# Kernel tuning notes

Hardware: AMD Instinct MI355X
Metric: run time of the kernel (lower is better)

Reference implementation:

```python
import jax, jax.numpy as jnp
import numpy as np

B, S, D = 1, 2048, 2048
H, KV, HD = 16, 4, 128
E, TOPK, F = 8, 2, 2048
THETA = 500000.0
CLIP = 8.0
EPS = 1e-5


def setup_inputs() -> dict:
    key = jax.random.key(0)
    ks = jax.random.split(key, 8)
    sc = 0.02
    return {
        "hidden_states": jax.random.normal(ks[0], (B, S, D), jnp.float32),
        "position_ids": jnp.arange(S, dtype=jnp.int64)[None, :].repeat(B, axis=0),
        "ln1_w": jnp.ones((D,), jnp.float32),
        "ln2_w": jnp.ones((D,), jnp.float32),
        "wqkv": jax.random.normal(ks[1], (D, (H + 2 * KV) * HD), jnp.float32) * sc,
        "wo": jax.random.normal(ks[2], (H * HD, D), jnp.float32) * sc,
        "router_w": jax.random.normal(ks[3], (E, D), jnp.float32) * sc,
        "w1": jax.random.normal(ks[4], (E, D, F), jnp.float32) * sc,
        "v1": jax.random.normal(ks[5], (E, D, F), jnp.float32) * sc,
        "w2": jax.random.normal(ks[6], (E, F, D), jnp.float32) * sc,
    }


def _layernorm(x, w):
    mu = jnp.mean(x, axis=-1, keepdims=True)
    var = jnp.mean((x - mu) ** 2, axis=-1, keepdims=True)
    return (x - mu) * jax.lax.rsqrt(var + EPS) * w


def _rotate_half(x):
    x1, x2 = jnp.split(x, 2, axis=-1)
    return jnp.concatenate([-x2, x1], axis=-1)


def _rope(pos):
    inv_freq = 1.0 / (THETA ** (jnp.arange(0, HD, 2, dtype=jnp.float32) / HD))
    ang = pos.astype(jnp.float32)[..., None] * inv_freq  # [B,S,HD/2]
    ang = jnp.concatenate([ang, ang], axis=-1)  # [B,S,HD]
    return jnp.cos(ang)[:, None], jnp.sin(ang)[:, None]  # [B,1,S,HD]


def _forward(hidden_states, position_ids, ln1_w, ln2_w, wqkv, wo, router_w, w1, v1, w2):
    x = hidden_states
    # --- attention sublayer ---
    h = _layernorm(x, ln1_w)
    qkv = jnp.clip(h @ wqkv, -CLIP, CLIP)  # [B,S,(H+2KV)*HD]
    q, k, v = jnp.split(qkv, [H * HD, (H + KV) * HD], axis=-1)
    q = q.reshape(B, S, H, HD).transpose(0, 2, 1, 3)   # [B,H,S,HD]
    k = k.reshape(B, S, KV, HD).transpose(0, 2, 1, 3)  # [B,KV,S,HD]
    v = v.reshape(B, S, KV, HD).transpose(0, 2, 1, 3)
    cos, sin = _rope(position_ids)
    q = q * cos + _rotate_half(q) * sin
    k = k * cos + _rotate_half(k) * sin
    rep = H // KV
    k = jnp.repeat(k, rep, axis=1)  # [B,H,S,HD]
    v = jnp.repeat(v, rep, axis=1)
    scores = jnp.einsum("bhqd,bhkd->bhqk", q, k) / np.sqrt(HD).astype(np.float32)
    causal = jnp.tril(jnp.ones((S, S), bool))
    scores = jnp.where(causal, scores, jnp.finfo(scores.dtype).min)
    probs = jax.nn.softmax(scores, axis=-1)
    attn = jnp.einsum("bhqk,bhkd->bhqd", probs, v)
    attn = attn.transpose(0, 2, 1, 3).reshape(B, S, H * HD) @ wo
    x = x + attn
    # --- MoE FFN sublayer ---
    h = _layernorm(x, ln2_w).reshape(B * S, D)  # [T,D]
    logits = h @ router_w.T                      # [T,E]
    rp = jax.nn.softmax(logits, axis=-1)
    top_w, top_i = jax.lax.top_k(rp, TOPK)       # [T,K]
    top_w = top_w / jnp.sum(top_w, axis=-1, keepdims=True)
    T = B * S
    gate = jnp.zeros((T, E), h.dtype).at[jnp.arange(T)[:, None], top_i].add(top_w)
    g = jax.nn.silu(jnp.einsum("td,edf->tef", h, w1)) * jnp.einsum("td,edf->tef", h, v1)
    y = jnp.einsum("tef,efd,te->td", g, w2, gate)
    x = x + y.reshape(B, S, D)
    return x


def reference(hidden_states, position_ids, ln1_w, ln2_w, wqkv, wo, router_w, w1, v1, w2):
    return _forward(hidden_states, position_ids, ln1_w, ln2_w, wqkv, wo, router_w, w1, v1, w2)
```

## Files before the change

kernel.cpp:

```cpp
#include <hip/hip_runtime.h>

#define S_LEN 2048
#define DMODEL 2048
#define NH 16
#define NKV 4
#define HD 128
#define NE 8
#define FF 2048
#define QKV_N 3072

typedef __attribute__((ext_vector_type(8))) short short8;
typedef __attribute__((ext_vector_type(4))) float f32x4;

__device__ inline unsigned short f2bf(float f) {
  unsigned int u = __builtin_bit_cast(unsigned int, f);
  u += 0x7fffu + ((u >> 16) & 1u);
  return (unsigned short)(u >> 16);
}
__device__ inline float bf2f(unsigned short h) {
  unsigned int u = ((unsigned int)h) << 16;
  return __builtin_bit_cast(float, u);
}
__device__ inline void split2(float v, unsigned short& h, unsigned short& l) {
  h = f2bf(v);
  l = f2bf(v - bf2f(h));
}


__device__ inline void stage_rows(const unsigned short* __restrict__ src, int ld,
                                  long row0, int k0, unsigned short* dst) {
  int t = threadIdx.x;
  int r = t >> 2, q = t & 3;
  int s = (r ^ (r >> 2)) & 3;
  uint4 v0 = *(const uint4*)(src + (size_t)(row0 + r) * ld + k0 + q * 8);
  uint4 v1 = *(const uint4*)(src + (size_t)(row0 + r + 64) * ld + k0 + q * 8);
  *(uint4*)(dst + r * 32 + ((q ^ s) << 3)) = v0;
  *(uint4*)(dst + (r + 64) * 32 + ((q ^ s) << 3)) = v1;
}

__device__ inline void loadA2_rows(const unsigned short* __restrict__ src, int ld,
                                   long row0, int k0, uint4 va[2]) {
  int t = threadIdx.x;
  int r = t >> 2, q = t & 3;
  va[0] = *(const uint4*)(src + (size_t)(row0 + r) * ld + k0 + q * 8);
  va[1] = *(const uint4*)(src + (size_t)(row0 + r + 64) * ld + k0 + q * 8);
}
__device__ inline void loadA2_g(const unsigned short* __restrict__ src, int ld,
                                const int* __restrict__ toks, int nvalid, int k0,
                                uint4 va[2]) {
  int t = threadIdx.x;
  int r = t >> 2, q = t & 3;
#pragma unroll
  for (int rr = 0; rr < 2; rr++) {
    int row = r + rr * 64;
    uint4 v = make_uint4(0, 0, 0, 0);
    if (row < nvalid) v = *(const uint4*)(src + (size_t)toks[row] * ld + k0 + q * 8);
    va[rr] = v;
  }
}
__device__ inline void writeA2(const uint4 va[2], unsigned short* dst) {
  int t = threadIdx.x;
  int r = t >> 2, q = t & 3;
  int s = (r ^ (r >> 2)) & 3;
  *(uint4*)(dst + r * 32 + ((q ^ s) << 3)) = va[0];
  *(uint4*)(dst + (r + 64) * 32 + ((q ^ s) << 3)) = va[1];
}

__device__ inline void gload16(const void* g, void* l) {
  __builtin_amdgcn_global_load_lds((const __attribute__((address_space(1))) unsigned int*)g,
                                   (__attribute__((address_space(3))) unsigned int*)l,
                                   16, 0, 0);
}
__device__ inline void stageB_chunk(const unsigned short* __restrict__ chunk,
                                    unsigned short* __restrict__ lds) {
  int w = threadIdx.x >> 6, l = threadIdx.x & 63;
  const unsigned short* s = chunk + w * 1024 + l * 8;
  unsigned short* d = lds + w * 1024;
  gload16(s, d);
  gload16(s + 512, d + 512);
}

#define WAIT_ALL  asm volatile("s_waitcnt vmcnt(0) lgkmcnt(0)" ::: "memory")
#define WAIT_LDS  asm volatile("s_waitcnt lgkmcnt(0)" ::: "memory")
#define SCHEDBAR  __builtin_amdgcn_sched_barrier(0)
#define BAR       __builtin_amdgcn_s_barrier()


__device__ inline void mma16(const unsigned short* As, const unsigned short* Bs,
                             int wr, int wc, f32x4 acc[4][4]) {
  int l = threadIdx.x & 63;
  int lr = l & 15, lg = l >> 4;
  int qoff = ((lg ^ ((lr ^ (lr >> 2)) & 3)) << 3);
  short8 a[4], b[4];
#pragma unroll
  for (int m = 0; m < 4; m++)
    a[m] = *(const short8*)(As + (wr + m * 16 + lr) * 32 + qoff);
#pragma unroll
  for (int n = 0; n < 4; n++)
    b[n] = *(const short8*)(Bs + (wc + n * 16 + lr) * 32 + qoff);
#pragma unroll
  for (int m = 0; m < 4; m++)
#pragma unroll
    for (int n = 0; n < 4; n++)
      acc[m][n] = __builtin_amdgcn_mfma_f32_16x16x32_bf16(a[m], b[n], acc[m][n], 0, 0, 0);
}

__device__ inline void mma16_dualB(const unsigned short* As, const unsigned short* Bs1,
                                   const unsigned short* Bs2, int wr, int wc,
                                   f32x4 acc1[4][4], f32x4 acc2[4][4]) {
  int l = threadIdx.x & 63;
  int lr = l & 15, lg = l >> 4;
  int qoff = ((lg ^ ((lr ^ (lr >> 2)) & 3)) << 3);
  short8 a[4], b1[4], b2[4];
#pragma unroll
  for (int m = 0; m < 4; m++)
    a[m] = *(const short8*)(As + (wr + m * 16 + lr) * 32 + qoff);
#pragma unroll
  for (int n = 0; n < 4; n++) {
    b1[n] = *(const short8*)(Bs1 + (wc + n * 16 + lr) * 32 + qoff);
    b2[n] = *(const short8*)(Bs2 + (wc + n * 16 + lr) * 32 + qoff);
  }
#pragma unroll
  for (int m = 0; m < 4; m++)
#pragma unroll
    for (int n = 0; n < 4; n++) {
      acc1[m][n] = __builtin_amdgcn_mfma_f32_16x16x32_bf16(a[m], b1[n], acc1[m][n], 0, 0, 0);
      acc2[m][n] = __builtin_amdgcn_mfma_f32_16x16x32_bf16(a[m], b2[n], acc2[m][n], 0, 0, 0);
    }
}

__device__ inline void mma16_split_reg(const unsigned short* Ash, const unsigned short* Asl,
                                       const unsigned short* Bsh, const unsigned short* Bsl,
                                       int wr, int wc, f32x4 acc[4][4]) {
  int l = threadIdx.x & 63;
  int lr = l & 15, lg = l >> 4;
  int qoff = ((lg ^ ((lr ^ (lr >> 2)) & 3)) << 3);
  short8 ah[4], al[4], bh[4], bl[4];
#pragma unroll
  for (int m = 0; m < 4; m++) {
    ah[m] = *(const short8*)(Ash + (wr + m * 16 + lr) * 32 + qoff);
    al[m] = *(const short8*)(Asl + (wr + m * 16 + lr) * 32 + qoff);
  }
#pragma unroll
  for (int n = 0; n < 4; n++) {
    bh[n] = *(const short8*)(Bsh + (wc + n * 16 + lr) * 32 + qoff);
    bl[n] = *(const short8*)(Bsl + (wc + n * 16 + lr) * 32 + qoff);
  }
#pragma unroll
  for (int m = 0; m < 4; m++)
#pragma unroll
    for (int n = 0; n < 4; n++) {
      acc[m][n] = __builtin_amdgcn_mfma_f32_16x16x32_bf16(ah[m], bh[n], acc[m][n], 0, 0, 0);
      acc[m][n] = __builtin_amdgcn_mfma_f32_16x16x32_bf16(ah[m], bl[n], acc[m][n], 0, 0, 0);
      acc[m][n] = __builtin_amdgcn_mfma_f32_16x16x32_bf16(al[m], bh[n], acc[m][n], 0, 0, 0);
    }
}


__global__ __launch_bounds__(256) void k_pack1(const float* __restrict__ src, long ld,
                                               long zs, int nc,
                                               unsigned short* __restrict__ dst) {
  __shared__ float tile[32][132];
  const float* Sp = src + (long)blockIdx.z * zs;
  int c = blockIdx.x, t = threadIdx.x;
  for (int i = 0; i < 4; i++) {
    int kt = blockIdx.y * 4 + i;
    long k0 = (long)kt * 32, n0 = (long)c * 128;
    {
      int k = t >> 3, nn = (t & 7) * 16;
      const float4* p = (const float4*)(Sp + (k0 + k) * ld + n0 + nn);
#pragma unroll
      for (int j = 0; j < 4; j++) *(float4*)&tile[k][nn + j * 4] = p[j];
    }
    __syncthreads();
    size_t cbase = ((size_t)(blockIdx.z * nc + c) * 64 + kt) * 4096;
#pragma unroll
    for (int uu = 0; uu < 2; uu++) {
      int u = t * 2 + uu;
      int n = u >> 2, qp = u & 3;
      int q = qp ^ ((n ^ (n >> 2)) & 3);
      unsigned short hb[8] __attribute__((aligned(16)));
#pragma unroll
      for (int j = 0; j < 8; j++) hb[j] = f2bf(tile[8 * q + j][n]);
      *(uint4*)(dst + cbase + u * 8) = *(const uint4*)hb;
    }
    __syncthreads();
  }
}

__global__ __launch_bounds__(256) void k_pack2(const float* __restrict__ src, long ld,
                                               long zs, int nc,
                                               unsigned short* __restrict__ dh,
                                               unsigned short* __restrict__ dl) {
  __shared__ float tile[32][132];
  const float* Sp = src + (long)blockIdx.z * zs;
  int c = blockIdx.x, t = threadIdx.x;
  for (int i = 0; i < 4; i++) {
    int kt = blockIdx.y * 4 + i;
    long k0 = (long)kt * 32, n0 = (long)c * 128;
    {
      int k = t >> 3, nn = (t & 7) * 16;
      const float4* p = (const float4*)(Sp + (k0 + k) * ld + n0 + nn);
#pragma unroll
      for (int j = 0; j < 4; j++) *(float4*)&tile[k][nn + j * 4] = p[j];
    }
    __syncthreads();
    size_t cbase = ((size_t)(blockIdx.z * nc + c) * 64 + kt) * 4096;
#pragma unroll
    for (int uu = 0; uu < 2; uu++) {
      int u = t * 2 + uu;
      int n = u >> 2, qp = u & 3;
      int q = qp ^ ((n ^ (n >> 2)) & 3);
      unsigned short hb[8] __attribute__((aligned(16)));
      unsigned short lb[8] __attribute__((aligned(16)));
#pragma unroll
      for (int j = 0; j < 8; j++) split2(tile[8 * q + j][n], hb[j], lb[j]);
      *(uint4*)(dh + cbase + u * 8) = *(const uint4*)hb;
      *(uint4*)(dl + cbase + u * 8) = *(const uint4*)lb;
    }
    __syncthreads();
  }
}

__global__ __launch_bounds__(256) void k_packbf(const unsigned short* __restrict__ src,
                                                unsigned short* __restrict__ dst) {
  int ttile = blockIdx.x;
  int z = blockIdx.y;
  const unsigned short* Sp = src + ((size_t)z * S_LEN + (size_t)ttile * 128) * HD;
  size_t ob = ((size_t)z * 64 + (size_t)ttile * 4) * 4096;
  int t = threadIdx.x;
#pragma unroll
  for (int kst = 0; kst < 4; kst++) {
#pragma unroll
    for (int uu = 0; uu < 2; uu++) {
      int u = t * 2 + uu;
      int n = u >> 2, qp = u & 3;
      int q = qp ^ ((n ^ (n >> 2)) & 3);
      *(uint4*)(dst + ob + (size_t)kst * 4096 + u * 8) =
          *(const uint4*)(Sp + (size_t)n * HD + kst * 32 + q * 8);
    }
  }
}


__global__ __launch_bounds__(256) void k_qkv_s(const unsigned short* __restrict__ Ah,
                                               const unsigned short* __restrict__ Al,
                                               const unsigned short* __restrict__ BPh,
                                               const unsigned short* __restrict__ BPl,
                                               float* __restrict__ C) {
  __shared__ unsigned short Ash[2 * 4096], Asl[2 * 4096], Bsh[2 * 4096], Bsl[2 * 4096];
  int row0 = blockIdx.y * 128;
  size_t cb = (size_t)blockIdx.x * 64 * 4096;
  int w = threadIdx.x >> 6;
  int wr = (w >> 1) * 64, wc = (w & 1) * 64;
  uint4 vah[2], val[2];
  loadA2_rows(Ah, DMODEL, row0, 0, vah);
  loadA2_rows(Al, DMODEL, row0, 0, val);
  stageB_chunk(BPh + cb, Bsh);
  stageB_chunk(BPl + cb, Bsl);
  writeA2(vah, Ash);
  writeA2(val, Asl);
  WAIT_ALL;
  BAR;
  f32x4 acc[4][4] = {};
  for (int kt = 0; kt < 64; kt++) {
    int cur = (kt & 1) << 12, nxt = 4096 - cur;
    if (kt + 1 < 64) {
      loadA2_rows(Ah, DMODEL, row0, (kt + 1) * 32, vah);
      loadA2_rows(Al, DMODEL, row0, (kt + 1) * 32, val);
      stageB_chunk(BPh + cb + (size_t)(kt + 1) * 4096, Bsh + nxt);
      stageB_chunk(BPl + cb + (size_t)(kt + 1) * 4096, Bsl + nxt);
    }
    SCHEDBAR;
    mma16_split_reg(Ash + cur, Asl + cur, Bsh + cur, Bsl + cur, wr, wc, acc);
    SCHEDBAR;
    if (kt + 1 < 64) {
      writeA2(vah, Ash + nxt);
      writeA2(val, Asl + nxt);
    }
    WAIT_ALL;
    BAR;
  }
  int col0 = blockIdx.x * 128;
  int l = threadIdx.x & 63;
  int er = wr + ((l >> 4) << 2), ec = wc + (l & 15);
#pragma unroll
  for (int m = 0; m < 4; m++)
#pragma unroll
    for (int n = 0; n < 4; n++)
#pragma unroll
      for (int r = 0; r < 4; r++) {
        float v = acc[m][n][r];
        v = fminf(fmaxf(v, -8.f), 8.f);
        C[(size_t)(row0 + er + m * 16 + r) * QKV_N + col0 + ec + n * 16] = v;
      }
}

__global__ __launch_bounds__(256) void k_wo_s(const unsigned short* __restrict__ Ah,
                                              const unsigned short* __restrict__ Al,
                                              const unsigned short* __restrict__ BPh,
                                              const unsigned short* __restrict__ BPl,
                                              const float* __restrict__ resid,
                                              float* __restrict__ x1) {
  __shared__ unsigned short Ash[2 * 4096], Asl[2 * 4096], Bsh[2 * 4096], Bsl[2 * 4096];
  int row0 = blockIdx.y * 128;
  size_t cb = (size_t)blockIdx.x * 64 * 4096;
  int w = threadIdx.x >> 6;
  int wr = (w >> 1) * 64, wc = (w & 1) * 64;
  uint4 vah[2], val[2];
  loadA2_rows(Ah, DMODEL, row0, 0, vah);
  loadA2_rows(Al, DMODEL, row0, 0, val);
  stageB_chunk(BPh + cb, Bsh);
  stageB_chunk(BPl + cb, Bsl);
  writeA2(vah, Ash);
  writeA2(val, Asl);
  WAIT_ALL;
  BAR;
  f32x4 acc[4][4] = {};
  for (int kt = 0; kt < 64; kt++) {
    int cur = (kt & 1) << 12, nxt = 4096 - cur;
    if (kt + 1 < 64) {
      loadA2_rows(Ah, DMODEL, row0, (kt + 1) * 32, vah);
      loadA2_rows(Al, DMODEL, row0, (kt + 1) * 32, val);
      stageB_chunk(BPh + cb + (size_t)(kt + 1) * 4096, Bsh + nxt);
      stageB_chunk(BPl + cb + (size_t)(kt + 1) * 4096, Bsl + nxt);
    }
    SCHEDBAR;
    mma16_split_reg(Ash + cur, Asl + cur, Bsh + cur, Bsl + cur, wr, wc, acc);
    SCHEDBAR;
    if (kt + 1 < 64) {
      writeA2(vah, Ash + nxt);
      writeA2(val, Asl + nxt);
    }
    WAIT_ALL;
    BAR;
  }
  int col0 = blockIdx.x * 128;
  int l = threadIdx.x & 63;
  int er = wr + ((l >> 4) << 2), ec = wc + (l & 15);
#pragma unroll
  for (int m = 0; m < 4; m++)
#pragma unroll
    for (int n = 0; n < 4; n++)
#pragma unroll
      for (int r = 0; r < 4; r++) {
        size_t idx = (size_t)(row0 + er + m * 16 + r) * DMODEL + col0 + ec + n * 16;
        x1[idx] = resid[idx] + acc[m][n][r];
      }
}


__global__ __launch_bounds__(128) void k_flash(const unsigned short* __restrict__ qh,
                                               const unsigned short* __restrict__ ql,
                                               const unsigned short* __restrict__ kPh,
                                               const unsigned short* __restrict__ kPl,
                                               const unsigned short* __restrict__ vPh,
                                               const unsigned short* __restrict__ vPl,
                                               unsigned short* __restrict__ ath,
                                               unsigned short* __restrict__ atl) {
  int bid = blockIdx.x;
  int h = (bid & 7) | ((bid >> 8) << 3);
  int rt = (bid >> 3) & 31;
  int kv = h >> 2;
  int ntiles = (rt >> 1) + 1;
  __shared__ float Pds[2][32 * 132];
  int t = threadIdx.x;
  int w = t >> 6, l = t & 63;
  int lr = l & 15, lg = l >> 4;
  int qoff = ((lg ^ ((lr ^ (lr >> 2)) & 3)) << 3);
  int wrow0 = rt * 64 + w * 32;
  const unsigned short* Qbh = qh + (size_t)h * S_LEN * HD;
  const unsigned short* Qbl = ql + (size_t)h * S_LEN * HD;
  const unsigned short* Kch = kPh + (size_t)kv * 64 * 4096;
  const unsigned short* Kcl = kPl + (size_t)kv * 64 * 4096;
  const unsigned short* Vch = vPh + (size_t)kv * 64 * 4096;
  const unsigned short* Vcl = vPl + (size_t)kv * 64 * 4096;
  float* Pw = &Pds[w][0];
  float mrun[2][4], lrun[2][4];
  f32x4 Oc[2][8];
#pragma unroll
  for (int m = 0; m < 2; m++)
#pragma unroll
    for (int r = 0; r < 4; r++) { mrun[m][r] = -3.4e38f; lrun[m][r] = 0.f; }
#pragma unroll
  for (int m = 0; m < 2; m++)
#pragma unroll
    for (int n = 0; n < 8; n++)
#pragma unroll
      for (int r = 0; r < 4; r++) Oc[m][n][r] = 0.f;
  const float scale = 0.08838834764831845f;

  for (int kt = 0; kt < ntiles; kt++) {
    f32x4 Sa[2][8];
#pragma unroll
    for (int m = 0; m < 2; m++)
#pragma unroll
      for (int n = 0; n < 8; n++)
#pragma unroll
        for (int r = 0; r < 4; r++) Sa[m][n][r] = 0.f;
#pragma unroll
    for (int kst = 0; kst < 4; kst++) {
      short8 qfh[2], qfl[2];
#pragma unroll
      for (int m = 0; m < 2; m++) {
        size_t o = (size_t)(wrow0 + m * 16 + lr) * HD + kst * 32 + lg * 8;
        qfh[m] = *(const short8*)(Qbh + o);
        qfl[m] = *(const short8*)(Qbl + o);
      }
      const unsigned short* Kh = Kch + (size_t)(kt * 4 + kst) * 4096;
      const unsigned short* Kl = Kcl + (size_t)(kt * 4 + kst) * 4096;
      short8 bh[8], bl[8];
#pragma unroll
      for (int n = 0; n < 8; n++) {
        bh[n] = *(const short8*)(Kh + (n * 16 + lr) * 32 + qoff);
        bl[n] = *(const short8*)(Kl + (n * 16 + lr) * 32 + qoff);
      }
#pragma unroll
      for (int m = 0; m < 2; m++)
#pragma unroll
        for (int n = 0; n < 8; n++) {
          Sa[m][n] = __builtin_amdgcn_mfma_f32_16x16x32_bf16(qfh[m], bh[n], Sa[m][n], 0, 0, 0);
          Sa[m][n] = __builtin_amdgcn_mfma_f32_16x16x32_bf16(qfh[m], bl[n], Sa[m][n], 0, 0, 0);
          Sa[m][n] = __builtin_amdgcn_mfma_f32_16x16x32_bf16(qfl[m], bh[n], Sa[m][n], 0, 0, 0);
        }
    }
#pragma unroll
    for (int m = 0; m < 2; m++)
#pragma unroll
      for (int r = 0; r < 4; r++) {
        int row = wrow0 + m * 16 + lg * 4 + r;
        float mx = mrun[m][r];
#pragma unroll
        for (int n = 0; n < 8; n++) {
          float v = Sa[m][n][r] * scale;
          int col = kt * 128 + n * 16 + lr;
          v = (col <= row) ? v : -3.4e38f;
          Sa[m][n][r] = v;
          mx = fmaxf(mx, v);
        }
        mx = fmaxf(mx, __shfl_xor(mx, 1));
        mx = fmaxf(mx, __shfl_xor(mx, 2));
        mx = fmaxf(mx, __shfl_xor(mx, 4));
        mx = fmaxf(mx, __shfl_xor(mx, 8));
        float al_ = expf(mrun[m][r] - mx);
        float sum = 0.f;
#pragma unroll
        for (int n = 0; n < 8; n++) {
          float v = Sa[m][n][r];
          float e = (v > -1.0e37f) ? expf(v - mx) : 0.f;
          Sa[m][n][r] = e;
          sum += e;
        }
        sum += __shfl_xor(sum, 1);
        sum += __shfl_xor(sum, 2);
        sum += __shfl_xor(sum, 4);
        sum += __shfl_xor(sum, 8);
        lrun[m][r] = lrun[m][r] * al_ + sum;
        mrun[m][r] = mx;
#pragma unroll
        for (int n = 0; n < 8; n++) Oc[m][n][r] *= al_;
      }
    WAIT_LDS;
    SCHEDBAR;
#pragma unroll
    for (int m = 0; m < 2; m++)
#pragma unroll
      for (int n = 0; n < 8; n++)
#pragma unroll
        for (int r = 0; r < 4; r++)
          Pw[(m * 16 + lg * 4 + r) * 132 + n * 16 + lr] = Sa[m][n][r];
    WAIT_LDS;
    SCHEDBAR;
#pragma unroll
    for (int kst = 0; kst < 4; kst++) {
      const unsigned short* Vh = Vch + (size_t)(kt * 4 + kst) * 4096;
      const unsigned short* Vl = Vcl + (size_t)(kt * 4 + kst) * 4096;
      short8 bh[8], bl[8];
#pragma unroll
      for (int n = 0; n < 8; n++) {
        bh[n] = *(const short8*)(Vh + (n * 16 + lr) * 32 + qoff);
        bl[n] = *(const short8*)(Vl + (n * 16 + lr) * 32 + qoff);
      }
#pragma unroll
      for (int m = 0; m < 2; m++) {
        const float* pp = &Pw[(m * 16 + lr) * 132 + kst * 32 + lg * 8];
        unsigned short ahb[8] __attribute__((aligned(16)));
        unsigned short alb[8] __attribute__((aligned(16)));
#pragma unroll
        for (int j = 0; j < 8; j++) split2(pp[j], ahb[j], alb[j]);
        short8 ah = *(const short8*)ahb;
        short8 al_ = *(const short8*)alb;
#pragma unroll
        for (int n = 0; n < 8; n++) {
          Oc[m][n] = __builtin_amdgcn_mfma_f32_16x16x32_bf16(ah, bh[n], Oc[m][n], 0, 0, 0);
          Oc[m][n] = __builtin_amdgcn_mfma_f32_16x16x32_bf16(ah, bl[n], Oc[m][n], 0, 0, 0);
          Oc[m][n] = __builtin_amdgcn_mfma_f32_16x16x32_bf16(al_, bh[n], Oc[m][n], 0, 0, 0);
        }
      }
    }
  }
#pragma unroll
  for (int m = 0; m < 2; m++)
#pragma unroll
    for (int r = 0; r < 4; r++) {
      size_t row = wrow0 + m * 16 + lg * 4 + r;
      float lv = lrun[m][r];
#pragma unroll
      for (int n = 0; n < 8; n++) {
        unsigned short hh, ll;
        split2(Oc[m][n][r] / lv, hh, ll);
        size_t o = row * DMODEL + (size_t)h * HD + n * 16 + lr;
        ath[o] = hh;
        atl[o] = ll;
      }
    }
}


__global__ __launch_bounds__(256) void k_moe1f(const unsigned short* __restrict__ h2b,
                                               const unsigned short* __restrict__ wPa,
                                               const unsigned short* __restrict__ wPb,
                                               const int* __restrict__ off,
                                               const int* __restrict__ ptok,
                                               const int* __restrict__ meta,
                                               unsigned short* __restrict__ g) {
  int ty = blockIdx.y;
  if (ty >= meta[25]) return;
  int tt = meta[26 + ty];
  int e = tt & 7, m0 = tt >> 3;
  int nvalid = min(128, meta[e] - m0);
  const int* toks = ptok + off[e] + m0;
  const unsigned short* B1 = wPa + (size_t)(e * 16 + blockIdx.x) * 64 * 4096;
  const unsigned short* B2 = wPb + (size_t)(e * 16 + blockIdx.x) * 64 * 4096;
  __shared__ unsigned short As[2 * 4096], Bs1[2 * 4096], Bs2[2 * 4096];
  int w = threadIdx.x >> 6;
  int wr = (w >> 1) * 64, wc = (w & 1) * 64;
  uint4 va[2];
  loadA2_g(h2b, DMODEL, toks, nvalid, 0, va);
  stageB_chunk(B1, Bs1);
  stageB_chunk(B2, Bs2);
  writeA2(va, As);
  WAIT_ALL;
  BAR;
  f32x4 acc1[4][4] = {}, acc2[4][4] = {};
  for (int kt = 0; kt < 64; kt++) {
    int cur = (kt & 1) << 12, nxt = 4096 - cur;
    if (kt + 1 < 64) {
      loadA2_g(h2b, DMODEL, toks, nvalid, (kt + 1) * 32, va);
      stageB_chunk(B1 + (size_t)(kt + 1) * 4096, Bs1 + nxt);
      stageB_chunk(B2 + (size_t)(kt + 1) * 4096, Bs2 + nxt);
    }
    SCHEDBAR;
    mma16_dualB(As + cur, Bs1 + cur, Bs2 + cur, wr, wc, acc1, acc2);
    SCHEDBAR;
    if (kt + 1 < 64) writeA2(va, As + nxt);
    WAIT_ALL;
    BAR;
  }
  int col0 = blockIdx.x * 128;
  int l = threadIdx.x & 63;
  int er = wr + ((l >> 4) << 2), ec = wc + (l & 15);
  size_t gbase = (size_t)off[e] + m0;
#pragma unroll
  for (int m = 0; m < 4; m++)
#pragma unroll
    for (int n = 0; n < 4; n++)
#pragma unroll
      for (int r = 0; r < 4; r++) {
        int rl = er + m * 16 + r;
        if (rl < nvalid) {
          float a = acc1[m][n][r];
          float s = a / (1.f + expf(-a));
          g[(gbase + rl) * FF + col0 + ec + n * 16] = f2bf(s * acc2[m][n][r]);
        }
      }
}

__global__ __launch_bounds__(256) void k_moe2(const unsigned short* __restrict__ g,
                                              const unsigned short* __restrict__ wP,
                                              const int* __restrict__ off,
                                              const int* __restrict__ ptok,
                                              const float* __restrict__ pw,
                                              const int* __restrict__ meta,
                                              float* __restrict__ y) {
  int ty = blockIdx.y;
  if (ty >= meta[25]) return;
  int tt = meta[26 + ty];
  int e = tt & 7, m0 = tt >> 3;
  int nvalid = min(128, meta[e] - m0);
  long pbase = (long)off[e] + m0;
  const unsigned short* Bb = wP + (size_t)(e * 16 + blockIdx.x) * 64 * 4096;
  __shared__ unsigned short As[2 * 4096], Bs[2 * 4096];
  int w = threadIdx.x >> 6;
  int wr = (w >> 1) * 64, wc = (w & 1) * 64;
  uint4 va[2];
  loadA2_rows(g, FF, pbase, 0, va);
  stageB_chunk(Bb, Bs);
  writeA2(va, As);
  WAIT_ALL;
  BAR;
  f32x4 acc[4][4] = {};
  for (int kt = 0; kt < 64; kt++) {
    int cur = (kt & 1) << 12, nxt = 4096 - cur;
    if (kt + 1 < 64) {
      loadA2_rows(g, FF, pbase, (kt + 1) * 32, va);
      stageB_chunk(Bb + (size_t)(kt + 1) * 4096, Bs + nxt);
    }
    SCHEDBAR;
    mma16(As + cur, Bs + cur, wr, wc, acc);
    SCHEDBAR;
    if (kt + 1 < 64) writeA2(va, As + nxt);
    WAIT_ALL;
    BAR;
  }
  int col0 = blockIdx.x * 128;
  int l = threadIdx.x & 63;
  int er = wr + ((l >> 4) << 2), ec = wc + (l & 15);
#pragma unroll
  for (int m = 0; m < 4; m++)
#pragma unroll
    for (int n = 0; n < 4; n++)
#pragma unroll
      for (int r = 0; r < 4; r++) {
        int rl = er + m * 16 + r;
        if (rl < nvalid) {
          long p = pbase + rl;
          int tk = ptok[p];
          atomicAdd(&y[(size_t)tk * DMODEL + col0 + ec + n * 16], acc[m][n][r] * pw[p]);
        }
      }
}


__global__ __launch_bounds__(256) void k_ln(const float* __restrict__ x,
                                            const float* __restrict__ w,
                                            unsigned short* __restrict__ obh,
                                            unsigned short* __restrict__ obl,
                                            float* __restrict__ of) {
  int row = blockIdx.x;
  const float* xr = x + (size_t)row * DMODEL;
  float s = 0.f, ss = 0.f;
  for (int c = threadIdx.x; c < DMODEL; c += 256) {
    float v = xr[c];
    s += v; ss += v * v;
  }
#pragma unroll
  for (int o = 32; o; o >>= 1) { s += __shfl_down(s, o); ss += __shfl_down(ss, o); }
  __shared__ float rs[4], rss[4], mu_s, inv_s;
  int wid = threadIdx.x >> 6;
  if ((threadIdx.x & 63) == 0) { rs[wid] = s; rss[wid] = ss; }
  __syncthreads();
  if (threadIdx.x == 0) {
    float S1 = rs[0] + rs[1] + rs[2] + rs[3];
    float S2 = rss[0] + rss[1] + rss[2] + rss[3];
    float mu = S1 / DMODEL;
    mu_s = mu;
    inv_s = rsqrtf(S2 / DMODEL - mu * mu + 1e-5f);
  }
  __syncthreads();
  float mu = mu_s, inv = inv_s;
  for (int c = threadIdx.x; c < DMODEL; c += 256) {
    float v = (xr[c] - mu) * inv * w[c];
    unsigned short hh, ll;
    split2(v, hh, ll);
    obh[(size_t)row * DMODEL + c] = hh;
    if (obl) obl[(size_t)row * DMODEL + c] = ll;
    if (of) of[(size_t)row * DMODEL + c] = v;
  }
}

__global__ void k_rope2(const float* __restrict__ qkv, unsigned short* __restrict__ qh,
                        unsigned short* __restrict__ ql, unsigned short* __restrict__ kh,
                        unsigned short* __restrict__ kl) {
  int t = blockIdx.x;
  int d = threadIdx.x;
  float pf = (float)pow(500000.0, (double)d * (1.0 / 64.0));
  float invf = 1.0f / pf;
  float ang = (float)t * invf;
  float cs = (float)cos((double)ang);
  float sn = (float)sin((double)ang);
  const float* row = qkv + (size_t)t * QKV_N;
  unsigned short hh, ll;
#pragma unroll
  for (int hq = 0; hq < NH; hq++) {
    float a = row[hq * HD + d], b = row[hq * HD + d + 64];
    size_t base = ((size_t)hq * S_LEN + t) * HD;
    split2(a * cs - b * sn, hh, ll); qh[base + d] = hh; ql[base + d] = ll;
    split2(b * cs + a * sn, hh, ll); qh[base + d + 64] = hh; ql[base + d + 64] = ll;
  }
#pragma unroll
  for (int kv = 0; kv < NKV; kv++) {
    float a = row[NH * HD + kv * HD + d], b = row[NH * HD + kv * HD + d + 64];
    size_t base = ((size_t)kv * S_LEN + t) * HD;
    split2(a * cs - b * sn, hh, ll); kh[base + d] = hh; kl[base + d] = ll;
    split2(b * cs + a * sn, hh, ll); kh[base + d + 64] = hh; kl[base + d + 64] = ll;
  }
}

__global__ __launch_bounds__(256) void k_router(const float* __restrict__ h2,
                                                const float* __restrict__ rw,
                                                int* __restrict__ topi,
                                                float* __restrict__ topw,
                                                int* __restrict__ cnt) {
  int t = blockIdx.x;
  __shared__ float hs[DMODEL];
  __shared__ float lg[NE];
  for (int c = threadIdx.x; c < DMODEL; c += 256) hs[c] = h2[(size_t)t * DMODEL + c];
  __syncthreads();
  int grp = threadIdx.x >> 5;
  int ln = threadIdx.x & 31;
  float p = 0.f;
  for (int c = ln; c < DMODEL; c += 32) p += hs[c] * rw[(size_t)grp * DMODEL + c];
#pragma unroll
  for (int o = 16; o; o >>= 1) p += __shfl_down(p, o, 32);
  if (ln == 0) lg[grp] = p;
  __syncthreads();
  if (threadIdx.x == 0) {
    float l0 = -3.4e38f; int i0 = 0;
    for (int e = 0; e < NE; e++)
      if (lg[e] > l0) { l0 = lg[e]; i0 = e; }
    float l1 = -3.4e38f; int i1 = 0;
    for (int e = 0; e < NE; e++)
      if (e != i0 && lg[e] > l1) { l1 = lg[e]; i1 = e; }
    float z = expf(l1 - l0);
    topi[t * 2] = i0; topi[t * 2 + 1] = i1;
    topw[t * 2] = 1.f / (1.f + z); topw[t * 2 + 1] = z / (1.f + z);
    atomicAdd(&cnt[i0], 1);
    atomicAdd(&cnt[i1], 1);
  }
}

__global__ void k_scan(int* __restrict__ meta) {
  if (threadIdx.x == 0 && blockIdx.x == 0) {
    int o = 0, nt = 0;
    for (int e = 0; e < NE; e++) {
      meta[16 + e] = o;
      for (int m0 = 0; m0 < meta[e]; m0 += 128) meta[26 + nt++] = (m0 << 3) | e;
      o += meta[e];
    }
    meta[24] = o;
    meta[25] = nt;
  }
}

__global__ void k_fill(const int* __restrict__ topi, const float* __restrict__ topw,
                       int* __restrict__ meta, int* __restrict__ ptok,
                       float* __restrict__ pw) {
  int t = blockIdx.x * blockDim.x + threadIdx.x;
  if (t >= S_LEN) return;
#pragma unroll
  for (int j = 0; j < 2; j++) {
    int e = topi[t * 2 + j];
    int p = atomicAdd(&meta[8 + e], 1);
    ptok[meta[16 + e] + p] = t;
    pw[meta[16 + e] + p] = topw[t * 2 + j];
  }
}

__global__ void k_final(float* __restrict__ out, const float* __restrict__ y) {
  int i = blockIdx.x * blockDim.x + threadIdx.x;
  float4 a = ((const float4*)out)[i];
  float4 b = ((const float4*)y)[i];
  ((float4*)out)[i] = make_float4(a.x + b.x, a.y + b.y, a.z + b.z, a.w + b.w);
}


extern "C" void kernel_launch(void* const* d_in, const int* in_sizes, int n_in,
                              void* d_out, int out_size, void* d_ws, size_t ws_size,
                              hipStream_t stream) {
  (void)in_sizes; (void)n_in; (void)out_size; (void)ws_size;
  const float* x = (const float*)d_in[0];
  const float* ln1w = (const float*)d_in[2];
  const float* ln2w = (const float*)d_in[3];
  const float* wqkv = (const float*)d_in[4];
  const float* wo = (const float*)d_in[5];
  const float* rw = (const float*)d_in[6];
  const float* w1 = (const float*)d_in[7];
  const float* v1 = (const float*)d_in[8];
  const float* w2 = (const float*)d_in[9];
  float* out = (float*)d_out;

  char* wsb = (char*)d_ws;
  const size_t MiB = 1u << 20;
  unsigned short* h1h = (unsigned short*)(wsb + 0 * MiB);
  unsigned short* h1l = (unsigned short*)(wsb + 8 * MiB);
  float* qkvb = (float*)(wsb + 16 * MiB);
  unsigned short* qh = (unsigned short*)(wsb + 40 * MiB);
  unsigned short* ql = (unsigned short*)(wsb + 48 * MiB);
  unsigned short* kh = (unsigned short*)(wsb + 56 * MiB);
  unsigned short* kl = (unsigned short*)(wsb + 58 * MiB);
  unsigned short* vPh = (unsigned short*)(wsb + 60 * MiB);
  unsigned short* vPl = (unsigned short*)(wsb + 62 * MiB);
  unsigned short* kPh = (unsigned short*)(wsb + 64 * MiB);
  unsigned short* kPl = (unsigned short*)(wsb + 66 * MiB);
  unsigned short* ath = (unsigned short*)(wsb + 68 * MiB);
  unsigned short* atl = (unsigned short*)(wsb + 76 * MiB);
  unsigned short* wqkvPh = (unsigned short*)(wsb + 84 * MiB);
  unsigned short* wqkvPl = (unsigned short*)(wsb + 96 * MiB);
  unsigned short* woPh = (unsigned short*)(wsb + 108 * MiB);
  unsigned short* woPl = (unsigned short*)(wsb + 116 * MiB);
  float* h2f = (float*)(wsb + 0 * MiB);
  unsigned short* h2b = (unsigned short*)(wsb + 16 * MiB);
  unsigned short* g = (unsigned short*)(wsb + 24 * MiB);
  float* y = (float*)(wsb + 40 * MiB);
  unsigned short* wPa = (unsigned short*)(wsb + 56 * MiB);
  unsigned short* wPb = (unsigned short*)(wsb + 120 * MiB);
  char* small = wsb + 184 * MiB;
  int* topi = (int*)small;
  float* topw = (float*)(small + 16384);
  int* ptok = (int*)(small + 32768);
  float* pw = (float*)(small + 49152);
  int* meta = (int*)(small + 65536);

  k_pack2<<<dim3(QKV_N / 128, 16, 1), 256, 0, stream>>>(wqkv, QKV_N, 0, QKV_N / 128,
                                                        wqkvPh, wqkvPl);
  k_pack2<<<dim3(DMODEL / 128, 16, 1), 256, 0, stream>>>(wo, DMODEL, 0, DMODEL / 128,
                                                         woPh, woPl);

  k_ln<<<S_LEN, 256, 0, stream>>>(x, ln1w, h1h, h1l, (float*)nullptr);
  k_qkv_s<<<dim3(QKV_N / 128, S_LEN / 128), 256, 0, stream>>>(h1h, h1l, wqkvPh, wqkvPl, qkvb);
  k_rope2<<<S_LEN, 64, 0, stream>>>(qkvb, qh, ql, kh, kl);
  k_pack2<<<dim3(1, 16, NKV), 256, 0, stream>>>(qkvb + (NH + NKV) * HD, QKV_N, HD, 1,
                                                vPh, vPl);
  k_packbf<<<dim3(16, NKV), 256, 0, stream>>>(kh, kPh);
  k_packbf<<<dim3(16, NKV), 256, 0, stream>>>(kl, kPl);
  k_flash<<<512, 128, 0, stream>>>(qh, ql, kPh, kPl, vPh, vPl, ath, atl);
  k_wo_s<<<dim3(16, 16), 256, 0, stream>>>(ath, atl, woPh, woPl, x, out);

  k_ln<<<S_LEN, 256, 0, stream>>>(out, ln2w, h2b, (unsigned short*)nullptr, h2f);
  hipMemsetAsync(y, 0, (size_t)S_LEN * DMODEL * 4, stream);
  hipMemsetAsync(meta, 0, 512, stream);
  k_router<<<S_LEN, 256, 0, stream>>>(h2f, rw, topi, topw, meta);
  k_scan<<<1, 64, 0, stream>>>(meta);
  k_fill<<<8, 256, 0, stream>>>(topi, topw, meta, ptok, pw);
  k_pack1<<<dim3(16, 16, NE), 256, 0, stream>>>(w1, FF, (long)DMODEL * FF, 16, wPa);
  k_pack1<<<dim3(16, 16, NE), 256, 0, stream>>>(v1, FF, (long)DMODEL * FF, 16, wPb);
  k_moe1f<<<dim3(16, 40), 256, 0, stream>>>(h2b, wPa, wPb, meta + 16, ptok, meta, g);
  k_pack1<<<dim3(16, 16, NE), 256, 0, stream>>>(w2, DMODEL, (long)FF * DMODEL, 16, wPa);
  k_moe2<<<dim3(16, 40), 256, 0, stream>>>(g, wPa, meta + 16, ptok, pw, meta, y);
  k_final<<<(S_LEN * DMODEL / 4) / 256, 256, 0, stream>>>(out, y);
}
```

Before: 971.8 us.

## Pre-pack GEMM A operands into swizzled tiles and fold MoE output into residual

LayerNorm and flash attention now write their split bf16 outputs straight into the tiled, swizzled layout the GEMMs use. A new gather kernel packs routed tokens the same way, so every GEMM can stage A through direct global-to-LDS loads instead of register loads followed by LDS writes. The MoE GEMMs drop double buffering for a single buffer with two barriers per k-step. The second expert GEMM now atomically adds into the output, which removes the y memset and the final add kernel. In exchange there is an extra gather pass, a redundant second LayerNorm launch, and less load/compute overlap in the MoE loops.

```diff
diff --git a/kernel.cpp b/kernel.cpp
--- a/kernel.cpp
+++ b/kernel.cpp
@@ -26,45 +26,6 @@
   l = f2bf(v - bf2f(h));
 }
 
-
-__device__ inline void stage_rows(const unsigned short* __restrict__ src, int ld,
-                                  long row0, int k0, unsigned short* dst) {
-  int t = threadIdx.x;
-  int r = t >> 2, q = t & 3;
-  int s = (r ^ (r >> 2)) & 3;
-  uint4 v0 = *(const uint4*)(src + (size_t)(row0 + r) * ld + k0 + q * 8);
-  uint4 v1 = *(const uint4*)(src + (size_t)(row0 + r + 64) * ld + k0 + q * 8);
-  *(uint4*)(dst + r * 32 + ((q ^ s) << 3)) = v0;
-  *(uint4*)(dst + (r + 64) * 32 + ((q ^ s) << 3)) = v1;
-}
-
-__device__ inline void loadA2_rows(const unsigned short* __restrict__ src, int ld,
-                                   long row0, int k0, uint4 va[2]) {
-  int t = threadIdx.x;
-  int r = t >> 2, q = t & 3;
-  va[0] = *(const uint4*)(src + (size_t)(row0 + r) * ld + k0 + q * 8);
-  va[1] = *(const uint4*)(src + (size_t)(row0 + r + 64) * ld + k0 + q * 8);
-}
-__device__ inline void loadA2_g(const unsigned short* __restrict__ src, int ld,
-                                const int* __restrict__ toks, int nvalid, int k0,
-                                uint4 va[2]) {
-  int t = threadIdx.x;
-  int r = t >> 2, q = t & 3;
-#pragma unroll
-  for (int rr = 0; rr < 2; rr++) {
-    int row = r + rr * 64;
-    uint4 v = make_uint4(0, 0, 0, 0);
-    if (row < nvalid) v = *(const uint4*)(src + (size_t)toks[row] * ld + k0 + q * 8);
-    va[rr] = v;
-  }
-}
-__device__ inline void writeA2(const uint4 va[2], unsigned short* dst) {
-  int t = threadIdx.x;
-  int r = t >> 2, q = t & 3;
-  int s = (r ^ (r >> 2)) & 3;
-  *(uint4*)(dst + r * 32 + ((q ^ s) << 3)) = va[0];
-  *(uint4*)(dst + (r + 64) * 32 + ((q ^ s) << 3)) = va[1];
-}
 
 __device__ inline void gload16(const void* g, void* l) {
   __builtin_amdgcn_global_load_lds((const __attribute__((address_space(1))) unsigned int*)g,
@@ -242,46 +203,66 @@
   }
 }
 
-
-__global__ __launch_bounds__(256) void k_qkv_s(const unsigned short* __restrict__ Ah,
-                                               const unsigned short* __restrict__ Al,
+__global__ __launch_bounds__(256) void k_gpack(const unsigned short* __restrict__ h2b,
+                                               const int* __restrict__ ptok,
+                                               const int* __restrict__ meta,
+                                               unsigned short* __restrict__ hAP) {
+  int ty = blockIdx.x;
+  if (ty >= meta[25]) return;
+  int tt = meta[26 + ty];
+  int e = tt & 7, m0 = tt >> 3;
+  int nvalid = min(128, meta[e] - m0);
+  const int* toks = ptok + meta[16 + e] + m0;
+  int t = threadIdx.x;
+  int r = t >> 2, q = t & 3;
+  int s = (r ^ (r >> 2)) & 3;
+  for (int kt = blockIdx.y * 8; kt < blockIdx.y * 8 + 8; kt++) {
+    unsigned short* dst = hAP + ((size_t)ty * 64 + kt) * 4096;
+#pragma unroll
+    for (int rr = 0; rr < 2; rr++) {
+      int row = r + rr * 64;
+      uint4 v = make_uint4(0, 0, 0, 0);
+      if (row < nvalid)
+        v = *(const uint4*)(h2b + (size_t)toks[row] * DMODEL + kt * 32 + q * 8);
+      *(uint4*)(dst + row * 32 + ((q ^ s) << 3)) = v;
+    }
+  }
+}
+
+
+__global__ __launch_bounds__(256) void k_qkv_s(const unsigned short* __restrict__ APh,
+                                               const unsigned short* __restrict__ APl,
                                                const unsigned short* __restrict__ BPh,
                                                const unsigned short* __restrict__ BPl,
                                                float* __restrict__ C) {
   __shared__ unsigned short Ash[2 * 4096], Asl[2 * 4096], Bsh[2 * 4096], Bsl[2 * 4096];
-  int row0 = blockIdx.y * 128;
+  size_t ab = (size_t)blockIdx.y * 64 * 4096;
   size_t cb = (size_t)blockIdx.x * 64 * 4096;
   int w = threadIdx.x >> 6;
   int wr = (w >> 1) * 64, wc = (w & 1) * 64;
-  uint4 vah[2], val[2];
-  loadA2_rows(Ah, DMODEL, row0, 0, vah);
-  loadA2_rows(Al, DMODEL, row0, 0, val);
+  stageB_chunk(APh + ab, Ash);
+  stageB_chunk(APl + ab, Asl);
   stageB_chunk(BPh + cb, Bsh);
   stageB_chunk(BPl + cb, Bsl);
-  writeA2(vah, Ash);
-  writeA2(val, Asl);
   WAIT_ALL;
   BAR;
   f32x4 acc[4][4] = {};
   for (int kt = 0; kt < 64; kt++) {
     int cur = (kt & 1) << 12, nxt = 4096 - cur;
     if (kt + 1 < 64) {
-      loadA2_rows(Ah, DMODEL, row0, (kt + 1) * 32, vah);
-      loadA2_rows(Al, DMODEL, row0, (kt + 1) * 32, val);
-      stageB_chunk(BPh + cb + (size_t)(kt + 1) * 4096, Bsh + nxt);
-      stageB_chunk(BPl + cb + (size_t)(kt + 1) * 4096, Bsl + nxt);
+      size_t o = (size_t)(kt + 1) * 4096;
+      stageB_chunk(APh + ab + o, Ash + nxt);
+      stageB_chunk(APl + ab + o, Asl + nxt);
+      stageB_chunk(BPh + cb + o, Bsh + nxt);
+      stageB_chunk(BPl + cb + o, Bsl + nxt);
     }
     SCHEDBAR;
     mma16_split_reg(Ash + cur, Asl + cur, Bsh + cur, Bsl + cur, wr, wc, acc);
     SCHEDBAR;
-    if (kt + 1 < 64) {
-      writeA2(vah, Ash + nxt);
-      writeA2(val, Asl + nxt);
-    }
     WAIT_ALL;
     BAR;
   }
-  int col0 = blockIdx.x * 128;
+  int row0 = blockIdx.y * 128, col0 = blockIdx.x * 128;
   int l = threadIdx.x & 63;
   int er = wr + ((l >> 4) << 2), ec = wc + (l & 15);
 #pragma unroll
@@ -296,46 +277,40 @@
       }
 }
 
-__global__ __launch_bounds__(256) void k_wo_s(const unsigned short* __restrict__ Ah,
-                                              const unsigned short* __restrict__ Al,
+__global__ __launch_bounds__(256) void k_wo_s(const unsigned short* __restrict__ APh,
+                                              const unsigned short* __restrict__ APl,
                                               const unsigned short* __restrict__ BPh,
                                               const unsigned short* __restrict__ BPl,
                                               const float* __restrict__ resid,
                                               float* __restrict__ x1) {
   __shared__ unsigned short Ash[2 * 4096], Asl[2 * 4096], Bsh[2 * 4096], Bsl[2 * 4096];
-  int row0 = blockIdx.y * 128;
+  size_t ab = (size_t)blockIdx.y * 64 * 4096;
   size_t cb = (size_t)blockIdx.x * 64 * 4096;
   int w = threadIdx.x >> 6;
   int wr = (w >> 1) * 64, wc = (w & 1) * 64;
-  uint4 vah[2], val[2];
-  loadA2_rows(Ah, DMODEL, row0, 0, vah);
-  loadA2_rows(Al, DMODEL, row0, 0, val);
+  stageB_chunk(APh + ab, Ash);
+  stageB_chunk(APl + ab, Asl);
   stageB_chunk(BPh + cb, Bsh);
   stageB_chunk(BPl + cb, Bsl);
-  writeA2(vah, Ash);
-  writeA2(val, Asl);
   WAIT_ALL;
   BAR;
   f32x4 acc[4][4] = {};
   for (int kt = 0; kt < 64; kt++) {
     int cur = (kt & 1) << 12, nxt = 4096 - cur;
     if (kt + 1 < 64) {
-      loadA2_rows(Ah, DMODEL, row0, (kt + 1) * 32, vah);
-      loadA2_rows(Al, DMODEL, row0, (kt + 1) * 32, val);
-      stageB_chunk(BPh + cb + (size_t)(kt + 1) * 4096, Bsh + nxt);
-      stageB_chunk(BPl + cb + (size_t)(kt + 1) * 4096, Bsl + nxt);
+      size_t o = (size_t)(kt + 1) * 4096;
+      stageB_chunk(APh + ab + o, Ash + nxt);
+      stageB_chunk(APl + ab + o, Asl + nxt);
+      stageB_chunk(BPh + cb + o, Bsh + nxt);
+      stageB_chunk(BPl + cb + o, Bsl + nxt);
     }
     SCHEDBAR;
     mma16_split_reg(Ash + cur, Asl + cur, Bsh + cur, Bsl + cur, wr, wc, acc);
     SCHEDBAR;
-    if (kt + 1 < 64) {
-      writeA2(vah, Ash + nxt);
-      writeA2(val, Asl + nxt);
-    }
     WAIT_ALL;
     BAR;
   }
-  int col0 = blockIdx.x * 128;
+  int row0 = blockIdx.y * 128, col0 = blockIdx.x * 128;
   int l = threadIdx.x & 63;
   int er = wr + ((l >> 4) << 2), ec = wc + (l & 15);
 #pragma unroll
@@ -356,8 +331,8 @@
                                                const unsigned short* __restrict__ kPl,
                                                const unsigned short* __restrict__ vPh,
                                                const unsigned short* __restrict__ vPl,
-                                               unsigned short* __restrict__ ath,
-                                               unsigned short* __restrict__ atl) {
+                                               unsigned short* __restrict__ atPh,
+                                               unsigned short* __restrict__ atPl) {
   int bid = blockIdx.x;
   int h = (bid & 7) | ((bid >> 8) << 3);
   int rt = (bid >> 3) & 31;
@@ -503,25 +478,27 @@
   for (int m = 0; m < 2; m++)
 #pragma unroll
     for (int r = 0; r < 4; r++) {
-      size_t row = wrow0 + m * 16 + lg * 4 + r;
+      int row = wrow0 + m * 16 + lg * 4 + r;
+      int rtc = row >> 7, rl = row & 127;
+      int sr = (rl ^ (rl >> 2)) & 3;
       float lv = lrun[m][r];
 #pragma unroll
       for (int n = 0; n < 8; n++) {
+        int col = h * HD + n * 16 + lr;
+        size_t off = ((size_t)(rtc * 64 + (col >> 5))) * 4096 + rl * 32 +
+                     ((((col & 31) >> 3) ^ sr) << 3) + (col & 7);
         unsigned short hh, ll;
         split2(Oc[m][n][r] / lv, hh, ll);
-        size_t o = row * DMODEL + (size_t)h * HD + n * 16 + lr;
-        ath[o] = hh;
-        atl[o] = ll;
-      }
-    }
-}
-
-
-__global__ __launch_bounds__(256) void k_moe1f(const unsigned short* __restrict__ h2b,
+        atPh[off] = hh;
+        atPl[off] = ll;
+      }
+    }
+}
+
+
+__global__ __launch_bounds__(256) void k_moe1f(const unsigned short* __restrict__ hAP,
                                                const unsigned short* __restrict__ wPa,
                                                const unsigned short* __restrict__ wPb,
-                                               const int* __restrict__ off,
-                                               const int* __restrict__ ptok,
                                                const int* __restrict__ meta,
                                                unsigned short* __restrict__ g) {
   int ty = blockIdx.y;
@@ -529,38 +506,25 @@
   int tt = meta[26 + ty];
   int e = tt & 7, m0 = tt >> 3;
   int nvalid = min(128, meta[e] - m0);
-  const int* toks = ptok + off[e] + m0;
+  const unsigned short* Ab = hAP + (size_t)ty * 64 * 4096;
   const unsigned short* B1 = wPa + (size_t)(e * 16 + blockIdx.x) * 64 * 4096;
   const unsigned short* B2 = wPb + (size_t)(e * 16 + blockIdx.x) * 64 * 4096;
-  __shared__ unsigned short As[2 * 4096], Bs1[2 * 4096], Bs2[2 * 4096];
+  __shared__ unsigned short As[4096], Bs1[4096], Bs2[4096];
   int w = threadIdx.x >> 6;
   int wr = (w >> 1) * 64, wc = (w & 1) * 64;
-  uint4 va[2];
-  loadA2_g(h2b, DMODEL, toks, nvalid, 0, va);
-  stageB_chunk(B1, Bs1);
-  stageB_chunk(B2, Bs2);
-  writeA2(va, As);
-  WAIT_ALL;
-  BAR;
   f32x4 acc1[4][4] = {}, acc2[4][4] = {};
   for (int kt = 0; kt < 64; kt++) {
-    int cur = (kt & 1) << 12, nxt = 4096 - cur;
-    if (kt + 1 < 64) {
-      loadA2_g(h2b, DMODEL, toks, nvalid, (kt + 1) * 32, va);
-      stageB_chunk(B1 + (size_t)(kt + 1) * 4096, Bs1 + nxt);
-      stageB_chunk(B2 + (size_t)(kt + 1) * 4096, Bs2 + nxt);
-    }
-    SCHEDBAR;
-    mma16_dualB(As + cur, Bs1 + cur, Bs2 + cur, wr, wc, acc1, acc2);
-    SCHEDBAR;
-    if (kt + 1 < 64) writeA2(va, As + nxt);
-    WAIT_ALL;
-    BAR;
-  }
-  int col0 = blockIdx.x * 128;
+    __syncthreads();
+    size_t o = (size_t)kt * 4096;
+    stageB_chunk(Ab + o, As);
+    stageB_chunk(B1 + o, Bs1);
+    stageB_chunk(B2 + o, Bs2);
+    __syncthreads();
+    mma16_dualB(As, Bs1, Bs2, wr, wc, acc1, acc2);
+  }
   int l = threadIdx.x & 63;
   int er = wr + ((l >> 4) << 2), ec = wc + (l & 15);
-  size_t gbase = (size_t)off[e] + m0;
+  int ktf0 = blockIdx.x * 4;
 #pragma unroll
   for (int m = 0; m < 4; m++)
 #pragma unroll
@@ -568,50 +532,41 @@
 #pragma unroll
       for (int r = 0; r < 4; r++) {
         int rl = er + m * 16 + r;
-        if (rl < nvalid) {
-          float a = acc1[m][n][r];
-          float s = a / (1.f + expf(-a));
-          g[(gbase + rl) * FF + col0 + ec + n * 16] = f2bf(s * acc2[m][n][r]);
-        }
-      }
-}
-
-__global__ __launch_bounds__(256) void k_moe2(const unsigned short* __restrict__ g,
+        int cc = ec + n * 16;
+        float a = acc1[m][n][r];
+        float s = a / (1.f + expf(-a));
+        unsigned short val = (rl < nvalid) ? f2bf(s * acc2[m][n][r]) : (unsigned short)0;
+        int srl = (rl ^ (rl >> 2)) & 3;
+        g[((size_t)(ty * 64 + ktf0 + (cc >> 5))) * 4096 + rl * 32 +
+          ((((cc & 31) >> 3) ^ srl) << 3) + (cc & 7)] = val;
+      }
+}
+
+__global__ __launch_bounds__(256) void k_moe2(const unsigned short* __restrict__ gP,
                                               const unsigned short* __restrict__ wP,
-                                              const int* __restrict__ off,
                                               const int* __restrict__ ptok,
                                               const float* __restrict__ pw,
                                               const int* __restrict__ meta,
-                                              float* __restrict__ y) {
+                                              float* __restrict__ out) {
   int ty = blockIdx.y;
   if (ty >= meta[25]) return;
   int tt = meta[26 + ty];
   int e = tt & 7, m0 = tt >> 3;
   int nvalid = min(128, meta[e] - m0);
-  long pbase = (long)off[e] + m0;
+  long pbase = (long)meta[16 + e] + m0;
+  const unsigned short* Ab = gP + (size_t)ty * 64 * 4096;
   const unsigned short* Bb = wP + (size_t)(e * 16 + blockIdx.x) * 64 * 4096;
-  __shared__ unsigned short As[2 * 4096], Bs[2 * 4096];
+  __shared__ unsigned short As[4096], Bs[4096];
   int w = threadIdx.x >> 6;
   int wr = (w >> 1) * 64, wc = (w & 1) * 64;
-  uint4 va[2];
-  loadA2_rows(g, FF, pbase, 0, va);
-  stageB_chunk(Bb, Bs);
-  writeA2(va, As);
-  WAIT_ALL;
-  BAR;
   f32x4 acc[4][4] = {};
   for (int kt = 0; kt < 64; kt++) {
-    int cur = (kt & 1) << 12, nxt = 4096 - cur;
-    if (kt + 1 < 64) {
-      loadA2_rows(g, FF, pbase, (kt + 1) * 32, va);
-      stageB_chunk(Bb + (size_t)(kt + 1) * 4096, Bs + nxt);
-    }
-    SCHEDBAR;
-    mma16(As + cur, Bs + cur, wr, wc, acc);
-    SCHEDBAR;
-    if (kt + 1 < 64) writeA2(va, As + nxt);
-    WAIT_ALL;
-    BAR;
+    __syncthreads();
+    size_t o = (size_t)kt * 4096;
+    stageB_chunk(Ab + o, As);
+    stageB_chunk(Bb + o, Bs);
+    __syncthreads();
+    mma16(As, Bs, wr, wc, acc);
   }
   int col0 = blockIdx.x * 128;
   int l = threadIdx.x & 63;
@@ -626,7 +581,7 @@
         if (rl < nvalid) {
           long p = pbase + rl;
           int tk = ptok[p];
-          atomicAdd(&y[(size_t)tk * DMODEL + col0 + ec + n * 16], acc[m][n][r] * pw[p]);
+          atomicAdd(&out[(size_t)tk * DMODEL + col0 + ec + n * 16], acc[m][n][r] * pw[p]);
         }
       }
 }
@@ -636,7 +591,7 @@
                                             const float* __restrict__ w,
                                             unsigned short* __restrict__ obh,
                                             unsigned short* __restrict__ obl,
-                                            float* __restrict__ of) {
+                                            float* __restrict__ of, int mode) {
   int row = blockIdx.x;
   const float* xr = x + (size_t)row * DMODEL;
   float s = 0.f, ss = 0.f;
@@ -659,13 +614,22 @@
   }
   __syncthreads();
   float mu = mu_s, inv = inv_s;
+  int rt = row >> 7, rl = row & 127;
+  int sw = (rl ^ (rl >> 2)) & 3;
   for (int c = threadIdx.x; c < DMODEL; c += 256) {
     float v = (xr[c] - mu) * inv * w[c];
     unsigned short hh, ll;
     split2(v, hh, ll);
-    obh[(size_t)row * DMODEL + c] = hh;
-    if (obl) obl[(size_t)row * DMODEL + c] = ll;
-    if (of) of[(size_t)row * DMODEL + c] = v;
+    if (mode) {
+      size_t off = ((size_t)(rt * 64 + (c >> 5))) * 4096 + rl * 32 +
+                   ((((c & 31) >> 3) ^ sw) << 3) + (c & 7);
+      obh[off] = hh;
+      obl[off] = ll;
+    } else {
+      obh[(size_t)row * DMODEL + c] = hh;
+      obl[(size_t)row * DMODEL + c] = ll;
+      of[(size_t)row * DMODEL + c] = v;
+    }
   }
 }
 
@@ -757,13 +721,6 @@
   }
 }
 
-__global__ void k_final(float* __restrict__ out, const float* __restrict__ y) {
-  int i = blockIdx.x * blockDim.x + threadIdx.x;
-  float4 a = ((const float4*)out)[i];
-  float4 b = ((const float4*)y)[i];
-  ((float4*)out)[i] = make_float4(a.x + b.x, a.y + b.y, a.z + b.z, a.w + b.w);
-}
-
 
 extern "C" void kernel_launch(void* const* d_in, const int* in_sizes, int n_in,
                               void* d_out, int out_size, void* d_ws, size_t ws_size,
@@ -782,8 +739,8 @@
 
   char* wsb = (char*)d_ws;
   const size_t MiB = 1u << 20;
-  unsigned short* h1h = (unsigned short*)(wsb + 0 * MiB);
-  unsigned short* h1l = (unsigned short*)(wsb + 8 * MiB);
+  unsigned short* h1Ph = (unsigned short*)(wsb + 0 * MiB);
+  unsigned short* h1Pl = (unsigned short*)(wsb + 8 * MiB);
   float* qkvb = (float*)(wsb + 16 * MiB);
   unsigned short* qh = (unsigned short*)(wsb + 40 * MiB);
   unsigned short* ql = (unsigned short*)(wsb + 48 * MiB);
@@ -793,19 +750,19 @@
   unsigned short* vPl = (unsigned short*)(wsb + 62 * MiB);
   unsigned short* kPh = (unsigned short*)(wsb + 64 * MiB);
   unsigned short* kPl = (unsigned short*)(wsb + 66 * MiB);
-  unsigned short* ath = (unsigned short*)(wsb + 68 * MiB);
-  unsigned short* atl = (unsigned short*)(wsb + 76 * MiB);
+  unsigned short* atPh = (unsigned short*)(wsb + 68 * MiB);
+  unsigned short* atPl = (unsigned short*)(wsb + 76 * MiB);
   unsigned short* wqkvPh = (unsigned short*)(wsb + 84 * MiB);
   unsigned short* wqkvPl = (unsigned short*)(wsb + 96 * MiB);
   unsigned short* woPh = (unsigned short*)(wsb + 108 * MiB);
   unsigned short* woPl = (unsigned short*)(wsb + 116 * MiB);
-  float* h2f = (float*)(wsb + 0 * MiB);
-  unsigned short* h2b = (unsigned short*)(wsb + 16 * MiB);
-  unsigned short* g = (unsigned short*)(wsb + 24 * MiB);
-  float* y = (float*)(wsb + 40 * MiB);
-  unsigned short* wPa = (unsigned short*)(wsb + 56 * MiB);
-  unsigned short* wPb = (unsigned short*)(wsb + 120 * MiB);
-  char* small = wsb + 184 * MiB;
+  unsigned short* hAP = (unsigned short*)(wsb + 0 * MiB);
+  unsigned short* g = (unsigned short*)(wsb + 20 * MiB);
+  float* h2f = (float*)(wsb + 40 * MiB);
+  unsigned short* h2b = (unsigned short*)(wsb + 56 * MiB);
+  unsigned short* wPa = (unsigned short*)(wsb + 40 * MiB);
+  unsigned short* wPb = (unsigned short*)(wsb + 104 * MiB);
+  char* small = wsb + 168 * MiB;
   int* topi = (int*)small;
   float* topw = (float*)(small + 16384);
   int* ptok = (int*)(small + 32768);
@@ -817,26 +774,27 @@
   k_pack2<<<dim3(DMODEL / 128, 16, 1), 256, 0, stream>>>(wo, DMODEL, 0, DMODEL / 128,
                                                          woPh, woPl);
 
-  k_ln<<<S_LEN, 256, 0, stream>>>(x, ln1w, h1h, h1l, (float*)nullptr);
-  k_qkv_s<<<dim3(QKV_N / 128, S_LEN / 128), 256, 0, stream>>>(h1h, h1l, wqkvPh, wqkvPl, qkvb);
+  k_ln<<<S_LEN, 256, 0, stream>>>(x, ln1w, h1Ph, h1Pl, (float*)nullptr, 1);
+  k_qkv_s<<<dim3(QKV_N / 128, S_LEN / 128), 256, 0, stream>>>(h1Ph, h1Pl, wqkvPh, wqkvPl,
+                                                              qkvb);
   k_rope2<<<S_LEN, 64, 0, stream>>>(qkvb, qh, ql, kh, kl);
   k_pack2<<<dim3(1, 16, NKV), 256, 0, stream>>>(qkvb + (NH + NKV) * HD, QKV_N, HD, 1,
                                                 vPh, vPl);
   k_packbf<<<dim3(16, NKV), 256, 0, stream>>>(kh, kPh);
   k_packbf<<<dim3(16, NKV), 256, 0, stream>>>(kl, kPl);
-  k_flash<<<512, 128, 0, stream>>>(qh, ql, kPh, kPl, vPh, vPl, ath, atl);
-  k_wo_s<<<dim3(16, 16), 256, 0, stream>>>(ath, atl, woPh, woPl, x, out);
-
-  k_ln<<<S_LEN, 256, 0, stream>>>(out, ln2w, h2b, (unsigned short*)nullptr, h2f);
-  hipMemsetAsync(y, 0, (size_t)S_LEN * DMODEL * 4, stream);
+  k_flash<<<512, 128, 0, stream>>>(qh, ql, kPh, kPl, vPh, vPl, atPh, atPl);
+  k_wo_s<<<dim3(16, 16), 256, 0, stream>>>(atPh, atPl, woPh, woPl, x, out);
+
+  k_ln<<<S_LEN, 256, 0, stream>>>(out, ln2w, h2b, h2b, h2f, 0);
+  k_ln<<<S_LEN, 256, 0, stream>>>(out, ln2w, h2b, (unsigned short*)(wsb + 20 * MiB), h2f, 0);
   hipMemsetAsync(meta, 0, 512, stream);
   k_router<<<S_LEN, 256, 0, stream>>>(h2f, rw, topi, topw, meta);
   k_scan<<<1, 64, 0, stream>>>(meta);
   k_fill<<<8, 256, 0, stream>>>(topi, topw, meta, ptok, pw);
+  k_gpack<<<dim3(40, 8), 256, 0, stream>>>(h2b, ptok, meta, hAP);
   k_pack1<<<dim3(16, 16, NE), 256, 0, stream>>>(w1, FF, (long)DMODEL * FF, 16, wPa);
   k_pack1<<<dim3(16, 16, NE), 256, 0, stream>>>(v1, FF, (long)DMODEL * FF, 16, wPb);
-  k_moe1f<<<dim3(16, 40), 256, 0, stream>>>(h2b, wPa, wPb, meta + 16, ptok, meta, g);
+  k_moe1f<<<dim3(16, 40), 256, 0, stream>>>(hAP, wPa, wPb, meta, g);
   k_pack1<<<dim3(16, 16, NE), 256, 0, stream>>>(w2, DMODEL, (long)FF * DMODEL, 16, wPa);
-  k_moe2<<<dim3(16, 40), 256, 0, stream>>>(g, wPa, meta + 16, ptok, pw, meta, y);
-  k_final<<<(S_LEN * DMODEL / 4) / 256, 256, 0, stream>>>(out, y);
-}
+  k_moe2<<<dim3(16, 40), 256, 0, stream>>>(g, wPa, ptok, pw, meta, out);
+}
```

Measured after the change: 1.002 ms. +3.1%, slower.
